# Kernel optimization log

Measured on AMD Instinct MI355X. Metric: run time of the kernel, lower is better.

The kernel has to match this reference:

```python
import jax, jax.numpy as jnp
import numpy as np

N = 120000   # nodes
E = 1200000  # edges
F_IN = 14    # PascalVOC-SP node features
H = 64       # args.hidden
C = 21       # num_classes
EPS = 1e-5


def _glorot(k, shape):
    fan_in = shape[0]
    return jax.random.normal(k, shape, jnp.float32) / np.sqrt(fan_in).astype(np.float32)


def setup_inputs() -> dict:
    key = jax.random.key(0)
    ks = jax.random.split(key, 16)
    inp = {}
    inp['x1'] = jax.random.normal(ks[0], (N, F_IN), jnp.float32)
    inp['edge_index'] = jax.random.randint(ks[1], (2, E), 0, N)
    dims = [(F_IN, H), (H, H), (H, H), (H, H)]
    i = 2
    for l, (din, dout) in enumerate(dims, 1):
        inp[f'Wn{l}'] = _glorot(ks[i], (din, dout)); i += 1
        inp[f'Wr{l}'] = _glorot(ks[i], (din, dout)); i += 1
        inp[f'b{l}'] = jnp.zeros((dout,), jnp.float32)
    for l in (1, 2, 3):
        inp[f'g{l}'] = jnp.ones((H,), jnp.float32)
        inp[f'be{l}'] = jnp.zeros((H,), jnp.float32)
    inp['Wm0'] = _glorot(ks[10], (H, H))
    inp['gm0'] = jnp.ones((H,), jnp.float32)
    inp['bem0'] = jnp.zeros((H,), jnp.float32)
    inp['Wm1'] = _glorot(ks[11], (H, H))
    inp['gm1'] = jnp.ones((H,), jnp.float32)
    inp['bem1'] = jnp.zeros((H,), jnp.float32)
    inp['Wm2'] = _glorot(ks[12], (H, C))
    inp['bm2'] = jnp.zeros((C,), jnp.float32)
    return inp


def _bn(x, g, b):
    # BatchNorm1d forward with batch statistics (train-mode normalization, biased var)
    m = x.mean(axis=0)
    v = x.var(axis=0)
    return (x - m) * jax.lax.rsqrt(v + EPS) * g + b


def _sage(x, src, dst, Wn, Wr, b):
    # PyG SAGEConv (mean aggr): out = mean_neighbors @ Wn + b + x @ Wr
    s = jax.ops.segment_sum(x[src], dst, num_segments=N)        # [N, d]
    cnt = jax.ops.segment_sum(jnp.ones((src.shape[0],), x.dtype), dst, num_segments=N)
    mean = s / jnp.maximum(cnt, 1.0)[:, None]
    return mean @ Wn + b + x @ Wr


def _lrelu(z):
    return jnp.where(z > 0, z, 0.01 * z)


def reference(x1, edge_index, Wn1, Wr1, b1, Wn2, Wr2, b2, Wn3, Wr3, b3, Wn4, Wr4, b4,
              g1, be1, g2, be2, g3, be3, Wm0, gm0, bem0, Wm1, gm1, bem1, Wm2, bm2):
    src, dst = edge_index[0], edge_index[1]
    x = _bn(_lrelu(_sage(x1, src, dst, Wn1, Wr1, b1)), g1, be1)   # conv1 + bano1 (dropout off)
    x = _bn(_lrelu(_sage(x, src, dst, Wn2, Wr2, b2)), g2, be2)    # conv2 + bano2
    x = _bn(jax.nn.relu(_sage(x, src, dst, Wn3, Wr3, b3)), g3, be3)  # conv3 + bano3
    x = _sage(x, src, dst, Wn4, Wr4, b4)                          # conv4
    # mlpRep: Linear(no bias)->BN->ReLU x2, then Linear(bias), no final act
    x = jax.nn.relu(_bn(x @ Wm0, gm0, bem0))
    x = jax.nn.relu(_bn(x @ Wm1, gm1, bem1))
    return x @ Wm2 + bm2
```

## Files before the change

### kernel.cpp

```cpp
#include <hip/hip_runtime.h>

constexpr int NN = 120000;
constexpr int EE = 1200000;
constexpr float EPSV = 1e-5f;
constexpr int NCBLK   = (NN + 127) / 128;
constexpr int NMFMABLK = NN / 64;
constexpr int ASTRIDE = 32;
constexpr int NSLOT = 64;

constexpr int BNODES  = 128;
constexpr int NBUCK   = (NN + BNODES - 1) / BNODES;
constexpr int BSTRIDE = 1536;
constexpr int EPB3    = 4096;
constexpr int NB3     = (EE + EPB3 - 1) / EPB3;
constexpr int NSTATF  = 5*NSLOT*128;

typedef __attribute__((ext_vector_type(8))) short bf8v;
typedef __attribute__((ext_vector_type(4))) float f4v;

__device__ __forceinline__ float bf2f(unsigned short u){
  union { unsigned i; float f; } v; v.i = ((unsigned)u) << 16; return v.f;
}
__device__ __forceinline__ unsigned short f2bf(float f){
  union { float f; unsigned i; } v; v.f = f;
  unsigned u = v.i;
  return (unsigned short)((u + 0x7FFFu + ((u >> 16) & 1u)) >> 16);
}
__device__ __forceinline__ unsigned pack2(float a, float b){
  return (unsigned)f2bf(a) | ((unsigned)f2bf(b) << 16);
}
__device__ __forceinline__ float act_f(float z, int ACT){
  if (ACT == 1) return z > 0.0f ? z : 0.01f*z;
  if (ACT == 2) return fmaxf(z, 0.0f);
  return z;
}
__device__ __forceinline__ void acc8(uint4 u, float& a0, float& a1, float& a2, float& a3,
                                     float& a4, float& a5, float& a6, float& a7){
  a0 += bf2f((unsigned short)(u.x & 0xFFFF)); a1 += bf2f((unsigned short)(u.x >> 16));
  a2 += bf2f((unsigned short)(u.y & 0xFFFF)); a3 += bf2f((unsigned short)(u.y >> 16));
  a4 += bf2f((unsigned short)(u.z & 0xFFFF)); a5 += bf2f((unsigned short)(u.z >> 16));
  a6 += bf2f((unsigned short)(u.w & 0xFFFF)); a7 += bf2f((unsigned short)(u.w >> 16));
}

__global__ __launch_bounds__(512) void k_bucket(const int* __restrict__ src, const int* __restrict__ dst,
                                                int* __restrict__ cursor, unsigned* __restrict__ bucketed,
                                                float* __restrict__ stats){
  __shared__ int hist[NBUCK];
  __shared__ int lstart[NBUCK];
  const int tid = threadIdx.x;
  const int e0  = blockIdx.x * EPB3;
  for (int i = blockIdx.x*512 + tid; i < NSTATF; i += NB3*512) stats[i] = 0.0f;
  for (int i = tid; i < NBUCK; i += 512) hist[i] = 0;
  __syncthreads();

  const bool full = (e0 + EPB3 <= EE);
  if (full){
    #pragma unroll 4
    for (int k = 0; k < EPB3/512; k++){
      int d = dst[e0 + k*512 + tid];
      atomicAdd(&hist[d >> 7], 1);
    }
  } else {
    #pragma unroll 1
    for (int k = 0; k < EPB3/512; k++){
      int e = e0 + k*512 + tid;
      if (e < EE){
        int d = dst[e];
        atomicAdd(&hist[d >> 7], 1);
      }
    }
  }
  __syncthreads();
  for (int i = tid; i < NBUCK; i += 512){
    int h = hist[i];
    lstart[i] = (h > 0) ? atomicAdd(&cursor[i], h) : 0;
  }
  __syncthreads();
  for (int i = tid; i < NBUCK; i += 512) hist[i] = 0;
  __syncthreads();
  #pragma unroll 1
  for (int k = 0; k < EPB3/512; k++){
    int e = e0 + k*512 + tid;
    if (e < EE){
      int d = dst[e];
      int s = src[e];
      int b = d >> 7;
      int r = atomicAdd(&hist[b], 1);
      int idx = lstart[b] + r;
      if (idx < BSTRIDE)
        bucketed[(size_t)b*BSTRIDE + idx] = ((unsigned)s << 7) | (unsigned)(d & 127);
    }
  }
}

__global__ __launch_bounds__(256) void k_buildadj(const unsigned* __restrict__ bucketed,
                                                  const int* __restrict__ cursor,
                                                  int* __restrict__ cnt, int* __restrict__ adj,
                                                  float* __restrict__ invdeg){
  __shared__ alignas(16) int ladj[BNODES*ASTRIDE];
  __shared__ int lcnt[BNODES];
  const int tid = threadIdx.x;
  const int b   = blockIdx.x;
  if (tid < BNODES) lcnt[tid] = 0;
  __syncthreads();
  const int tot = min(cursor[b], BSTRIDE);
  const unsigned* rp = bucketed + (size_t)b*BSTRIDE;
  for (int e = tid; e < tot; e += 256){
    unsigned rec = rp[e];
    int d = (int)(rec & 127u);
    int s = (int)(rec >> 7);
    int p = atomicAdd(&lcnt[d], 1);
    if (p < ASTRIDE) ladj[d*ASTRIDE + p] = s;
  }
  __syncthreads();
  int4* ap = (int4*)(adj + (size_t)b*BNODES*ASTRIDE);
  const int4* lp = (const int4*)ladj;
  #pragma unroll
  for (int i = 0; i < (BNODES*ASTRIDE/4)/256; i++)
    ap[i*256 + tid] = lp[i*256 + tid];
  if (tid < BNODES){
    int c = lcnt[tid];
    int n = b*BNODES + tid;
    cnt[n] = c;
    invdeg[n] = (c > 0) ? (1.0f/(float)c) : -1.0f;
  }
}

__global__ __launch_bounds__(256) void k_gather14(const float* __restrict__ x,
                                                  const int* __restrict__ cnt, const int* __restrict__ adj,
                                                  float* __restrict__ agg){
  const int lane = threadIdx.x & 63;
  const int f = lane & 15, g = lane >> 4;
  const int wave = blockIdx.x*4 + (threadIdx.x >> 6);
  const int nwav = gridDim.x*4;
  for (int n = wave; n < NN; n += nwav){
    int d = min(cnt[n], ASTRIDE);
    const int st = n*ASTRIDE;
    float acc = 0.0f;
    for (int j = g; j < d; j += 4){
      int s = adj[st+j];
      if (f < 14) acc += x[(size_t)s*14 + f];
    }
    acc += __shfl_down(acc, 32);
    acc += __shfl_down(acc, 16);
    if (lane < 14) agg[(size_t)n*14 + lane] = acc;
  }
}

__global__ __launch_bounds__(256) void k_prep_conv_frag(const float* __restrict__ Wn, const float* __restrict__ Wr,
                                                        const float* __restrict__ b, const float* __restrict__ statSlots,
                                                        const float* __restrict__ g, const float* __restrict__ be,
                                                        unsigned short* __restrict__ frag, float* __restrict__ bias2){
  __shared__ float sc[64], sh[64];
  int t = threadIdx.x;
  if (t < 64){
    float sum = 0.0f, sq = 0.0f;
    #pragma unroll 8
    for (int s = 0; s < NSLOT; s++){
      sum += statSlots[s*128 + t];
      sq  += statSlots[s*128 + 64 + t];
    }
    float m = sum * (1.0f/NN);
    float v = sq * (1.0f/NN) - m*m;
    float a = g[t] * rsqrtf(v + EPSV);
    sc[t] = a; sh[t] = be[t] - m*a;
  }
  __syncthreads();
  if (blockIdx.x == 0 && t < 64){
    float accB = b[t], accN = 0.0f;
    for (int k=0;k<64;k++){
      accB += sh[k]*Wr[k*64+t];
      accN += sh[k]*Wn[k*64+t];
    }
    bias2[t]      = accB;
    bias2[64 + t] = accN;
  }
  {
    int idx = blockIdx.x*256 + t;
    int j    = idx & 7;
    int lane = (idx >> 3) & 63;
    int kk   = (idx >> 9) & 1;
    int ct   = (idx >> 10) & 3;
    int mat  = (idx >> 12) & 1;
    int k    = kk*32 + (lane >> 4)*8 + j;
    int col  = ct*16 + (lane & 15);
    const float* W = mat ? Wr : Wn;
    frag[idx] = f2bf(sc[k] * W[k*64 + col]);
  }
}

__global__ __launch_bounds__(256) void k_prep_lin_frag(const float* __restrict__ W,
                                                       unsigned short* __restrict__ frag,
                                                       float* __restrict__ bias2,
                                                       const float* __restrict__ bnSlots,
                                                       float* __restrict__ bnRed){
  int t = threadIdx.x;
  if (blockIdx.x == 0 && t < 128){
    bias2[t] = 0.0f;
    if (bnSlots){
      float s = 0.0f;
      #pragma unroll 8
      for (int sl = 0; sl < NSLOT; sl++) s += bnSlots[sl*128 + t];
      bnRed[t] = s;
    }
  }
  {
    int idx = blockIdx.x*256 + t;
    int j    = idx & 7;
    int lane = (idx >> 3) & 63;
    int kk   = (idx >> 9) & 1;
    int ct   = (idx >> 10) & 3;
    int k    = kk*32 + (lane >> 4)*8 + j;
    int col  = ct*16 + (lane & 15);
    frag[idx] = f2bf(W[k*64 + col]);
  }
}

__global__ __launch_bounds__(64) void k_prep_aff(const float* __restrict__ st,
                                                 const float* __restrict__ g, const float* __restrict__ be,
                                                 float* __restrict__ aff){
  int t = threadIdx.x;
  float s = 0.0f, q = 0.0f;
  #pragma unroll 8
  for (int sl = 0; sl < NSLOT; sl++){
    s += st[sl*128 + t];
    q += st[sl*128 + 64 + t];
  }
  float m = s*(1.0f/NN);
  float v = q*(1.0f/NN) - m*m;
  float a = g[t]*rsqrtf(v+EPSV);
  aff[t]      = a;
  aff[64 + t] = be[t] - m*a;
}

template<int ACT, bool STATS>
__global__ __launch_bounds__(256, 1) void k_gmfma(const unsigned short* __restrict__ X,
                                                  const int* __restrict__ cnt, const int* __restrict__ adj,
                                                  const float* __restrict__ invdeg,
                                                  const unsigned short* __restrict__ frag,
                                                  const float* __restrict__ bias2,
                                                  unsigned short* __restrict__ out,
                                                  float* __restrict__ statsOut){
  __shared__ unsigned short sMean[64*72];
  __shared__ float sst[512];
  const int tid  = threadIdx.x;
  const int lane = tid & 63;
  const int wv   = tid >> 6;
  const int nb0  = blockIdx.x*64;

  {
    const int q8 = lane & 7;
    const int h8 = lane >> 3;
    #pragma unroll
    for (int t8 = 0; t8 < 2; t8++){
      const int row = wv*16 + h8*2 + t8;
      const int n   = nb0 + row;
      const int d   = min(cnt[n], ASTRIDE);
      const int st  = n*ASTRIDE;
      float a0=0,a1=0,a2=0,a3=0,a4=0,a5=0,a6=0,a7=0;
      int j = 0;
      for (; j + 7 < d; j += 8){
        int4 sa = *(const int4*)(adj + st + j);
        int4 sb = *(const int4*)(adj + st + j + 4);
        uint4 u0 = *(const uint4*)(X + (size_t)sa.x*64 + 8*q8);
        uint4 u1 = *(const uint4*)(X + (size_t)sa.y*64 + 8*q8);
        uint4 u2 = *(const uint4*)(X + (size_t)sa.z*64 + 8*q8);
        uint4 u3 = *(const uint4*)(X + (size_t)sa.w*64 + 8*q8);
        uint4 u4 = *(const uint4*)(X + (size_t)sb.x*64 + 8*q8);
        uint4 u5 = *(const uint4*)(X + (size_t)sb.y*64 + 8*q8);
        uint4 u6 = *(const uint4*)(X + (size_t)sb.z*64 + 8*q8);
        uint4 u7 = *(const uint4*)(X + (size_t)sb.w*64 + 8*q8);
        acc8(u0,a0,a1,a2,a3,a4,a5,a6,a7); acc8(u1,a0,a1,a2,a3,a4,a5,a6,a7);
        acc8(u2,a0,a1,a2,a3,a4,a5,a6,a7); acc8(u3,a0,a1,a2,a3,a4,a5,a6,a7);
        acc8(u4,a0,a1,a2,a3,a4,a5,a6,a7); acc8(u5,a0,a1,a2,a3,a4,a5,a6,a7);
        acc8(u6,a0,a1,a2,a3,a4,a5,a6,a7); acc8(u7,a0,a1,a2,a3,a4,a5,a6,a7);
      }
      for (; j + 3 < d; j += 4){
        int4 sa = *(const int4*)(adj + st + j);
        uint4 u0 = *(const uint4*)(X + (size_t)sa.x*64 + 8*q8);
        uint4 u1 = *(const uint4*)(X + (size_t)sa.y*64 + 8*q8);
        uint4 u2 = *(const uint4*)(X + (size_t)sa.z*64 + 8*q8);
        uint4 u3 = *(const uint4*)(X + (size_t)sa.w*64 + 8*q8);
        acc8(u0,a0,a1,a2,a3,a4,a5,a6,a7); acc8(u1,a0,a1,a2,a3,a4,a5,a6,a7);
        acc8(u2,a0,a1,a2,a3,a4,a5,a6,a7); acc8(u3,a0,a1,a2,a3,a4,a5,a6,a7);
      }
      for (; j < d; j++){
        int s = adj[st + j];
        uint4 u = *(const uint4*)(X + (size_t)s*64 + 8*q8);
        acc8(u,a0,a1,a2,a3,a4,a5,a6,a7);
      }
      float iv = fmaxf(invdeg[n], 0.0f);
      uint4 o;
      o.x = pack2(a0*iv, a1*iv);
      o.y = pack2(a2*iv, a3*iv);
      o.z = pack2(a4*iv, a5*iv);
      o.w = pack2(a6*iv, a7*iv);
      *(uint4*)(sMean + row*72 + 8*q8) = o;
    }
  }

  const bf8v* fp = (const bf8v*)frag;
  bf8v wn[4][2], wr[4][2];
  #pragma unroll
  for (int ct=0;ct<4;ct++){
    #pragma unroll
    for (int kk=0;kk<2;kk++){
      wn[ct][kk] = fp[((0*4+ct)*2+kk)*64 + lane];
      wr[ct][kk] = fp[((1*4+ct)*2+kk)*64 + lane];
    }
  }
  const int m  = lane & 15;
  const int kq = lane >> 4;
  const size_t arow = (size_t)(nb0 + wv*16 + m)*64;
  bf8v ax0 = *(const bf8v*)(X + arow + kq*8);
  bf8v ax1 = *(const bf8v*)(X + arow + 32 + kq*8);
  __syncthreads();
  bf8v am0 = *(const bf8v*)(sMean + (wv*16 + m)*72 + kq*8);
  bf8v am1 = *(const bf8v*)(sMean + (wv*16 + m)*72 + 32 + kq*8);

  f4v acc[4];
  #pragma unroll
  for (int ct=0;ct<4;ct++){
    f4v c = {0.0f,0.0f,0.0f,0.0f};
    c = __builtin_amdgcn_mfma_f32_16x16x32_bf16(am0, wn[ct][0], c, 0,0,0);
    c = __builtin_amdgcn_mfma_f32_16x16x32_bf16(am1, wn[ct][1], c, 0,0,0);
    c = __builtin_amdgcn_mfma_f32_16x16x32_bf16(ax0, wr[ct][0], c, 0,0,0);
    c = __builtin_amdgcn_mfma_f32_16x16x32_bf16(ax1, wr[ct][1], c, 0,0,0);
    acc[ct] = c;
  }

  const int col = lane & 15;
  float bb[4], bg[4];
  #pragma unroll
  for (int ct=0;ct<4;ct++){
    bb[ct] = bias2[ct*16 + col];
    bg[ct] = bias2[64 + ct*16 + col];
  }
  float ls[4] = {0,0,0,0}, lq[4] = {0,0,0,0};
  #pragma unroll
  for (int r=0;r<4;r++){
    const int node = nb0 + wv*16 + (lane>>4)*4 + r;
    float gadd = (invdeg[node] > 0.0f) ? 1.0f : 0.0f;
    #pragma unroll
    for (int ct=0;ct<4;ct++){
      float z = acc[ct][r] + bb[ct] + gadd * bg[ct];
      z = act_f(z, ACT);
      out[(size_t)node*64 + ct*16 + col] = f2bf(z);
      if (STATS){ ls[ct] += z; lq[ct] = fmaf(z, z, lq[ct]); }
    }
  }
  if constexpr (STATS){
    #pragma unroll
    for (int ct=0;ct<4;ct++){
      float s = ls[ct]; s += __shfl_down(s, 32); s += __shfl_down(s, 16);
      float q = lq[ct]; q += __shfl_down(q, 32); q += __shfl_down(q, 16);
      if (kq == 0){
        sst[wv*128 + ct*16 + col]      = s;
        sst[wv*128 + 64 + ct*16 + col] = q;
      }
    }
    __syncthreads();
    if (tid < 128){
      float v = sst[tid] + sst[128+tid] + sst[256+tid] + sst[384+tid];
      atomicAdd(&statsOut[(blockIdx.x & (NSLOT-1))*128 + tid], v);
    }
  }
}

template<int ACT, bool STATS, bool BNA>
__global__ __launch_bounds__(256, 1) void k_mfma_lin(const unsigned short* __restrict__ Ax,
                                                     const unsigned short* __restrict__ frag,
                                                     const float* __restrict__ bias2,
                                                     unsigned short* __restrict__ out,
                                                     float* __restrict__ statsOut,
                                                     const float* __restrict__ bnRed,
                                                     const float* __restrict__ bnG,
                                                     const float* __restrict__ bnB){
  __shared__ float sst[512];
  const int lane = threadIdx.x & 63;
  const int wv   = threadIdx.x >> 6;
  const int n0   = (blockIdx.x*4 + wv)*16;
  const int m    = lane & 15;
  const int kq   = lane >> 4;

  const bf8v* fp = (const bf8v*)frag;
  bf8v wr[4][2];
  #pragma unroll
  for (int ct=0;ct<4;ct++){
    #pragma unroll
    for (int kk=0;kk<2;kk++) wr[ct][kk] = fp[(ct*2+kk)*64 + lane];
  }

  const size_t arow = (size_t)(n0 + m)*64;
  bf8v ax0 = *(const bf8v*)(Ax + arow + kq*8);
  bf8v ax1 = *(const bf8v*)(Ax + arow + 32 + kq*8);
  if constexpr (BNA){
    #pragma unroll
    for (int j=0;j<8;j++){
      int k0 = kq*8 + j, k1 = 32 + kq*8 + j;
      float m0 = bnRed[k0]*(1.0f/NN);
      float v0 = bnRed[64+k0]*(1.0f/NN) - m0*m0;
      float a0 = bnG[k0]*rsqrtf(v0+EPSV);
      float b0 = bnB[k0] - m0*a0;
      ax0[j] = (short)f2bf(fmaxf(fmaf(a0, bf2f((unsigned short)ax0[j]), b0), 0.0f));
      float m1 = bnRed[k1]*(1.0f/NN);
      float v1 = bnRed[64+k1]*(1.0f/NN) - m1*m1;
      float a1 = bnG[k1]*rsqrtf(v1+EPSV);
      float b1 = bnB[k1] - m1*a1;
      ax1[j] = (short)f2bf(fmaxf(fmaf(a1, bf2f((unsigned short)ax1[j]), b1), 0.0f));
    }
  }

  f4v acc[4];
  #pragma unroll
  for (int ct=0;ct<4;ct++){
    f4v c = {0.0f,0.0f,0.0f,0.0f};
    c = __builtin_amdgcn_mfma_f32_16x16x32_bf16(ax0, wr[ct][0], c, 0,0,0);
    c = __builtin_amdgcn_mfma_f32_16x16x32_bf16(ax1, wr[ct][1], c, 0,0,0);
    acc[ct] = c;
  }

  const int col = lane & 15;
  float bb[4];
  #pragma unroll
  for (int ct=0;ct<4;ct++) bb[ct] = bias2[ct*16 + col];
  float ls[4] = {0,0,0,0}, lq[4] = {0,0,0,0};
  #pragma unroll
  for (int r=0;r<4;r++){
    const int node = n0 + (lane>>4)*4 + r;
    #pragma unroll
    for (int ct=0;ct<4;ct++){
      float z = act_f(acc[ct][r] + bb[ct], ACT);
      out[(size_t)node*64 + ct*16 + col] = f2bf(z);
      if (STATS){ ls[ct] += z; lq[ct] = fmaf(z, z, lq[ct]); }
    }
  }
  if constexpr (STATS){
    #pragma unroll
    for (int ct=0;ct<4;ct++){
      float s = ls[ct]; s += __shfl_down(s, 32); s += __shfl_down(s, 16);
      float q = lq[ct]; q += __shfl_down(q, 32); q += __shfl_down(q, 16);
      if (kq == 0){
        sst[wv*128 + ct*16 + col]      = s;
        sst[wv*128 + 64 + ct*16 + col] = q;
      }
    }
    __syncthreads();
    if (threadIdx.x < 128){
      float v = sst[threadIdx.x] + sst[128+threadIdx.x] + sst[256+threadIdx.x] + sst[384+threadIdx.x];
      atomicAdd(&statsOut[(blockIdx.x & (NSLOT-1))*128 + threadIdx.x], v);
    }
  }
}

__global__ __launch_bounds__(128, 1) void k_gemm_conv14(const float* __restrict__ agg, const float* __restrict__ x,
                                                        const float* __restrict__ invdeg,
                                                        const float* __restrict__ Wn, const float* __restrict__ Wr,
                                                        const float* __restrict__ b,
                                                        unsigned short* __restrict__ out, float* __restrict__ statsOut){
  constexpr int DIN = 14, RS = 15;
  __shared__ float sRow[128*RS];
  const int tid = threadIdx.x;
  const int lane = tid & 63;
  const int n0  = blockIdx.x*128;
  const int n   = n0 + tid;

  {
    const float* gp = agg + (size_t)n0*DIN;
    for (int i = tid; i < 128*DIN; i += 128){
      int r = i / DIN, c = i - r*DIN;
      sRow[r*RS + c] = (n0 + r < NN) ? gp[i] : 0.0f;
    }
  }
  __syncthreads();

  float accA0[32], accA1[32];
  #pragma unroll
  for (int jj=0;jj<32;jj++){ accA0[jj]=0.0f; accA1[jj]=0.0f; }

  #pragma unroll 1
  for (int k=0;k<DIN;k++){
    float rv = sRow[tid*RS + k];
    const float* wr = Wn + k*64;
    #pragma unroll
    for (int jj=0;jj<32;jj++) accA0[jj] = fmaf(wr[jj],    rv, accA0[jj]);
    #pragma unroll
    for (int jj=0;jj<32;jj++) accA1[jj] = fmaf(wr[32+jj], rv, accA1[jj]);
  }
  __syncthreads();
  {
    const float* gp = x + (size_t)n0*DIN;
    for (int i = tid; i < 128*DIN; i += 128){
      int r = i / DIN, c = i - r*DIN;
      sRow[r*RS + c] = (n0 + r < NN) ? gp[i] : 0.0f;
    }
  }
  __syncthreads();

  const bool valid = (n < NN);
  float iv = valid ? invdeg[n] : -1.0f;
  const bool gate = iv > 0.0f;
  #pragma unroll
  for (int jj=0;jj<32;jj++){
    accA0[jj] = gate ? accA0[jj]*iv : 0.0f;
    accA1[jj] = gate ? accA1[jj]*iv : 0.0f;
  }

  #pragma unroll 1
  for (int k=0;k<DIN;k++){
    float rv = sRow[tid*RS + k];
    const float* wr = Wr + k*64;
    #pragma unroll
    for (int jj=0;jj<32;jj++) accA0[jj] = fmaf(wr[jj],    rv, accA0[jj]);
    #pragma unroll
    for (int jj=0;jj<32;jj++) accA1[jj] = fmaf(wr[32+jj], rv, accA1[jj]);
  }

  uint2* o2 = (uint2*)(out + (size_t)n*64);
  float vs[64], vq[64];
  #pragma unroll
  for (int q=0;q<8;q++){
    float z0 = valid ? act_f(accA0[4*q+0]+b[4*q+0],1) : 0.0f;
    float z1 = valid ? act_f(accA0[4*q+1]+b[4*q+1],1) : 0.0f;
    float z2 = valid ? act_f(accA0[4*q+2]+b[4*q+2],1) : 0.0f;
    float z3 = valid ? act_f(accA0[4*q+3]+b[4*q+3],1) : 0.0f;
    vs[4*q+0] = z0; vs[4*q+1] = z1; vs[4*q+2] = z2; vs[4*q+3] = z3;
    if (valid){ uint2 t; t.x = pack2(z0,z1); t.y = pack2(z2,z3); o2[q] = t; }
  }
  #pragma unroll
  for (int q=0;q<8;q++){
    float z0 = valid ? act_f(accA1[4*q+0]+b[32+4*q+0],1) : 0.0f;
    float z1 = valid ? act_f(accA1[4*q+1]+b[32+4*q+1],1) : 0.0f;
    float z2 = valid ? act_f(accA1[4*q+2]+b[32+4*q+2],1) : 0.0f;
    float z3 = valid ? act_f(accA1[4*q+3]+b[32+4*q+3],1) : 0.0f;
    vs[32+4*q+0] = z0; vs[32+4*q+1] = z1; vs[32+4*q+2] = z2; vs[32+4*q+3] = z3;
    if (valid){ uint2 t; t.x = pack2(z0,z1); t.y = pack2(z2,z3); o2[8+q] = t; }
  }
  #pragma unroll
  for (int j=0;j<64;j++) vq[j] = vs[j]*vs[j];

  #pragma unroll
  for (int k=0;k<6;k++){
    const bool keep1 = ((lane >> k) & 1) != 0;
    const int half = 64 >> (k+1);
    #pragma unroll
    for (int i=0;i<half;i++){
      float sa = vs[2*i], sb = vs[2*i+1];
      float qa = vq[2*i], qb = vq[2*i+1];
      float skeep = keep1 ? sb : sa;
      float ssend = keep1 ? sa : sb;
      float qkeep = keep1 ? qb : qa;
      float qsend = keep1 ? qa : qb;
      vs[i] = skeep + __shfl_xor(ssend, 1<<k);
      vq[i] = qkeep + __shfl_xor(qsend, 1<<k);
    }
  }
  const int slot = (blockIdx.x & (NSLOT-1))*128;
  atomicAdd(&statsOut[slot + lane],      vs[0]);
  atomicAdd(&statsOut[slot + 64 + lane], vq[0]);
}

__global__ __launch_bounds__(256, 1) void k_lin21(const unsigned short* __restrict__ x,
                                                  const float* __restrict__ W, const float* __restrict__ bias,
                                                  const float* __restrict__ aff,
                                                  float* __restrict__ out){
  __shared__ float sW[64*21];
  __shared__ float sAff[128];
  const int tid = threadIdx.x;
  if (tid < 128) sAff[tid] = aff[tid];
  for (int i = tid; i < 64*21; i += 256) sW[i] = W[i];
  __syncthreads();

  const int p  = tid & 3;
  const int nl = tid >> 2;
  const int n  = blockIdx.x*64 + nl;
  const bool valid = (n < NN);
  const int k0 = p*16;

  uint4 u0 = {0,0,0,0}, u1 = {0,0,0,0};
  if (valid){
    const unsigned short* rp = x + (size_t)n*64 + k0;
    u0 = *(const uint4*)(rp);
    u1 = *(const uint4*)(rp + 8);
  }
  float f[16];
  f[0]=bf2f((unsigned short)(u0.x&0xFFFF)); f[1]=bf2f((unsigned short)(u0.x>>16));
  f[2]=bf2f((unsigned short)(u0.y&0xFFFF)); f[3]=bf2f((unsigned short)(u0.y>>16));
  f[4]=bf2f((unsigned short)(u0.z&0xFFFF)); f[5]=bf2f((unsigned short)(u0.z>>16));
  f[6]=bf2f((unsigned short)(u0.w&0xFFFF)); f[7]=bf2f((unsigned short)(u0.w>>16));
  f[8]=bf2f((unsigned short)(u1.x&0xFFFF)); f[9]=bf2f((unsigned short)(u1.x>>16));
  f[10]=bf2f((unsigned short)(u1.y&0xFFFF)); f[11]=bf2f((unsigned short)(u1.y>>16));
  f[12]=bf2f((unsigned short)(u1.z&0xFFFF)); f[13]=bf2f((unsigned short)(u1.z>>16));
  f[14]=bf2f((unsigned short)(u1.w&0xFFFF)); f[15]=bf2f((unsigned short)(u1.w>>16));
  #pragma unroll
  for (int j=0;j<16;j++)
    f[j] = fmaxf(fmaf(sAff[k0+j], f[j], sAff[64+k0+j]), 0.0f);

  float a[21];
  #pragma unroll
  for (int jj=0;jj<21;jj++) a[jj] = 0.0f;
  #pragma unroll
  for (int k=0;k<16;k++){
    const float* wr = sW + (k0+k)*21;
    float rv = f[k];
    #pragma unroll
    for (int jj=0;jj<21;jj++) a[jj] = fmaf(wr[jj], rv, a[jj]);
  }
  #pragma unroll
  for (int jj=0;jj<21;jj++){
    a[jj] += __shfl_xor(a[jj], 1);
    a[jj] += __shfl_xor(a[jj], 2);
  }
  if (valid){
    const int c0 = p*6;
    const int ce = (p == 3) ? 21 : c0 + 6;
    float* op = out + (size_t)n*21;
    #pragma unroll 6
    for (int jj=c0; jj<ce; jj++) op[jj] = a[jj] + bias[jj];
  }
}

extern "C" void kernel_launch(void* const* d_in, const int* in_sizes, int n_in,
                              void* d_out, int out_size, void* d_ws, size_t ws_size,
                              hipStream_t stream){
  const float* x1  = (const float*)d_in[0];
  const int*   ei  = (const int*)d_in[1];
  const int* srcp = ei;
  const int* dstp = ei + EE;
  const float *Wn1=(const float*)d_in[2],  *Wr1=(const float*)d_in[3],  *b1=(const float*)d_in[4];
  const float *Wn2=(const float*)d_in[5],  *Wr2=(const float*)d_in[6],  *b2=(const float*)d_in[7];
  const float *Wn3=(const float*)d_in[8],  *Wr3=(const float*)d_in[9],  *b3=(const float*)d_in[10];
  const float *Wn4=(const float*)d_in[11], *Wr4=(const float*)d_in[12], *b4=(const float*)d_in[13];
  const float *g1=(const float*)d_in[14], *be1=(const float*)d_in[15];
  const float *g2=(const float*)d_in[16], *be2=(const float*)d_in[17];
  const float *g3=(const float*)d_in[18], *be3=(const float*)d_in[19];
  const float *Wm0=(const float*)d_in[20], *gm0=(const float*)d_in[21], *bem0=(const float*)d_in[22];
  const float *Wm1=(const float*)d_in[23], *gm1=(const float*)d_in[24], *bem1=(const float*)d_in[25];
  const float *Wm2=(const float*)d_in[26], *bm2=(const float*)d_in[27];
  float* out = (float*)d_out;

  char* ws = (char*)d_ws;
  int*   cnt     = (int*)(ws);
  float* invdeg  = (float*)(ws + (1ull<<20));
  int*   adj     = (int*)(ws + (2ull<<20));
  float* agg14   = (float*)(ws + (18ull<<20));
  unsigned short* hA   = (unsigned short*)(ws + (25ull<<20));
  unsigned short* hB   = (unsigned short*)(ws + (41ull<<20));
  float* stats   = (float*)(ws + (57ull<<20));
  float* bnRed   = (float*)(ws + (57ull<<20) + 192*1024);
  float* aff5    = (float*)(ws + (57ull<<20) + 224*1024);
  unsigned short* fragC = (unsigned short*)(ws + (58ull<<20));
  float* bias2C  = (float*)(ws + (58ull<<20) + 65536);
  unsigned short* fragL = (unsigned short*)(ws + (59ull<<20));
  float* bias2L  = (float*)(ws + (59ull<<20) + 65536);
  unsigned* bucketed = (unsigned*)(ws + (25ull<<20));
  int* cursor        = (int*)(ws + (25ull<<20) + (6ull<<20));

  float* S1 = stats;
  float* S2 = stats + NSLOT*128;
  float* S3 = stats + 2*NSLOT*128;
  float* S4 = stats + 3*NSLOT*128;
  float* S5 = stats + 4*NSLOT*128;

  hipMemsetAsync(cursor, 0, NBUCK*sizeof(int), stream);
  k_bucket  <<<NB3,  512,0,stream>>>(srcp, dstp, cursor, bucketed, stats);
  k_buildadj<<<NBUCK,256,0,stream>>>(bucketed, cursor, cnt, adj, invdeg);

  k_gather14<<<2048,256,0,stream>>>(x1, cnt, adj, agg14);
  k_gemm_conv14<<<NCBLK,128,0,stream>>>(agg14,x1,invdeg,Wn1,Wr1,b1,hA,S1);

  k_prep_conv_frag<<<32,256,0,stream>>>(Wn2,Wr2,b2,S1,g1,be1,fragC,bias2C);
  k_gmfma<1,true><<<NMFMABLK,256,0,stream>>>(hA,cnt,adj,invdeg,fragC,bias2C,hB,S2);

  k_prep_conv_frag<<<32,256,0,stream>>>(Wn3,Wr3,b3,S2,g2,be2,fragC,bias2C);
  k_gmfma<2,true><<<NMFMABLK,256,0,stream>>>(hB,cnt,adj,invdeg,fragC,bias2C,hA,S3);

  k_prep_conv_frag<<<32,256,0,stream>>>(Wn4,Wr4,b4,S3,g3,be3,fragC,bias2C);
  k_gmfma<0,false><<<NMFMABLK,256,0,stream>>>(hA,cnt,adj,invdeg,fragC,bias2C,hB,nullptr);

  k_prep_lin_frag<<<16,256,0,stream>>>(Wm0, fragL, bias2L, nullptr, nullptr);
  k_mfma_lin<0,true,false><<<NMFMABLK,256,0,stream>>>(hB,fragL,bias2L,hA,S4,nullptr,nullptr,nullptr);

  k_prep_lin_frag<<<16,256,0,stream>>>(Wm1, fragL, bias2L, S4, bnRed);
  k_mfma_lin<0,true,true><<<NMFMABLK,256,0,stream>>>(hA,fragL,bias2L,hB,S5,bnRed,gm0,bem0);

  k_prep_aff<<<1,64,0,stream>>>(S5, gm1, bem1, aff5);
  k_lin21<<<NMFMABLK,256,0,stream>>>(hB,Wm2,bm2,aff5,out);
}
```

Before: 398.3 us.

## Fuse layer-1 neighbor gather into conv1 kernel using bf16-packed padded features

Converts the 14-wide fp32 input features to a padded bf16 layout of 32 bytes per row inside the bucketing kernel. The separate gather kernel is removed, and conv1 now does its own per-thread neighbor mean aggregation before the dense transform. This drops one launch and the agg14 intermediate round trip, and halves gather bytes. In exchange, each thread walks its node's adjacency serially, which may hurt latency hiding in a kernel limited to 128 threads with one block, and bf16 rounding of the input features lowers precision.

```diff
diff --git a/kernel.cpp b/kernel.cpp
--- a/kernel.cpp
+++ b/kernel.cpp
@@ -44,12 +44,20 @@
 
 __global__ __launch_bounds__(512) void k_bucket(const int* __restrict__ src, const int* __restrict__ dst,
                                                 int* __restrict__ cursor, unsigned* __restrict__ bucketed,
-                                                float* __restrict__ stats){
+                                                float* __restrict__ stats,
+                                                const float* __restrict__ x, unsigned* __restrict__ xb){
   __shared__ int hist[NBUCK];
   __shared__ int lstart[NBUCK];
   const int tid = threadIdx.x;
   const int e0  = blockIdx.x * EPB3;
   for (int i = blockIdx.x*512 + tid; i < NSTATF; i += NB3*512) stats[i] = 0.0f;
+  for (int i = blockIdx.x*512 + tid; i < NN*8; i += NB3*512){
+    int n = i >> 3, j = i & 7;
+    int c0 = 2*j, c1 = 2*j + 1;
+    float f0 = (c0 < 14) ? x[(size_t)n*14 + c0] : 0.0f;
+    float f1 = (c1 < 14) ? x[(size_t)n*14 + c1] : 0.0f;
+    xb[i] = pack2(f0, f1);
+  }
   for (int i = tid; i < NBUCK; i += 512) hist[i] = 0;
   __syncthreads();
 
@@ -123,27 +131,6 @@
     int n = b*BNODES + tid;
     cnt[n] = c;
     invdeg[n] = (c > 0) ? (1.0f/(float)c) : -1.0f;
-  }
-}
-
-__global__ __launch_bounds__(256) void k_gather14(const float* __restrict__ x,
-                                                  const int* __restrict__ cnt, const int* __restrict__ adj,
-                                                  float* __restrict__ agg){
-  const int lane = threadIdx.x & 63;
-  const int f = lane & 15, g = lane >> 4;
-  const int wave = blockIdx.x*4 + (threadIdx.x >> 6);
-  const int nwav = gridDim.x*4;
-  for (int n = wave; n < NN; n += nwav){
-    int d = min(cnt[n], ASTRIDE);
-    const int st = n*ASTRIDE;
-    float acc = 0.0f;
-    for (int j = g; j < d; j += 4){
-      int s = adj[st+j];
-      if (f < 14) acc += x[(size_t)s*14 + f];
-    }
-    acc += __shfl_down(acc, 32);
-    acc += __shfl_down(acc, 16);
-    if (lane < 14) agg[(size_t)n*14 + lane] = acc;
   }
 }
 
@@ -453,62 +440,71 @@
   }
 }
 
-__global__ __launch_bounds__(128, 1) void k_gemm_conv14(const float* __restrict__ agg, const float* __restrict__ x,
-                                                        const float* __restrict__ invdeg,
-                                                        const float* __restrict__ Wn, const float* __restrict__ Wr,
-                                                        const float* __restrict__ b,
-                                                        unsigned short* __restrict__ out, float* __restrict__ statsOut){
+__global__ __launch_bounds__(128, 1) void k_conv1(const unsigned* __restrict__ xb, const float* __restrict__ x,
+                                                  const int* __restrict__ cnt, const int* __restrict__ adj,
+                                                  const float* __restrict__ invdeg,
+                                                  const float* __restrict__ Wn, const float* __restrict__ Wr,
+                                                  const float* __restrict__ b,
+                                                  unsigned short* __restrict__ out, float* __restrict__ statsOut){
   constexpr int DIN = 14, RS = 15;
-  __shared__ float sRow[128*RS];
+  __shared__ float sMean[128*RS];
+  __shared__ float sX[128*RS];
   const int tid = threadIdx.x;
   const int lane = tid & 63;
   const int n0  = blockIdx.x*128;
   const int n   = n0 + tid;
-
-  {
-    const float* gp = agg + (size_t)n0*DIN;
-    for (int i = tid; i < 128*DIN; i += 128){
-      int r = i / DIN, c = i - r*DIN;
-      sRow[r*RS + c] = (n0 + r < NN) ? gp[i] : 0.0f;
-    }
-  }
-  __syncthreads();
-
-  float accA0[32], accA1[32];
-  #pragma unroll
-  for (int jj=0;jj<32;jj++){ accA0[jj]=0.0f; accA1[jj]=0.0f; }
-
-  #pragma unroll 1
-  for (int k=0;k<DIN;k++){
-    float rv = sRow[tid*RS + k];
-    const float* wr = Wn + k*64;
-    #pragma unroll
-    for (int jj=0;jj<32;jj++) accA0[jj] = fmaf(wr[jj],    rv, accA0[jj]);
-    #pragma unroll
-    for (int jj=0;jj<32;jj++) accA1[jj] = fmaf(wr[32+jj], rv, accA1[jj]);
-  }
-  __syncthreads();
+  const bool valid = (n < NN);
+
   {
     const float* gp = x + (size_t)n0*DIN;
     for (int i = tid; i < 128*DIN; i += 128){
       int r = i / DIN, c = i - r*DIN;
-      sRow[r*RS + c] = (n0 + r < NN) ? gp[i] : 0.0f;
-    }
-  }
-  __syncthreads();
-
-  const bool valid = (n < NN);
-  float iv = valid ? invdeg[n] : -1.0f;
-  const bool gate = iv > 0.0f;
-  #pragma unroll
-  for (int jj=0;jj<32;jj++){
-    accA0[jj] = gate ? accA0[jj]*iv : 0.0f;
-    accA1[jj] = gate ? accA1[jj]*iv : 0.0f;
-  }
+      sX[r*RS + c] = (n0 + r < NN) ? gp[i] : 0.0f;
+    }
+  }
+
+  {
+    float mm[14];
+    #pragma unroll
+    for (int j=0;j<14;j++) mm[j] = 0.0f;
+    const int d  = valid ? min(cnt[n], ASTRIDE) : 0;
+    const int st = n*ASTRIDE;
+    #pragma unroll 2
+    for (int j=0;j<d;j++){
+      int s = adj[st+j];
+      const uint4* rp = (const uint4*)(xb + s*8);
+      uint4 u0 = rp[0], u1 = rp[1];
+      mm[0]+=bf2f((unsigned short)(u0.x&0xFFFF)); mm[1]+=bf2f((unsigned short)(u0.x>>16));
+      mm[2]+=bf2f((unsigned short)(u0.y&0xFFFF)); mm[3]+=bf2f((unsigned short)(u0.y>>16));
+      mm[4]+=bf2f((unsigned short)(u0.z&0xFFFF)); mm[5]+=bf2f((unsigned short)(u0.z>>16));
+      mm[6]+=bf2f((unsigned short)(u0.w&0xFFFF)); mm[7]+=bf2f((unsigned short)(u0.w>>16));
+      mm[8]+=bf2f((unsigned short)(u1.x&0xFFFF)); mm[9]+=bf2f((unsigned short)(u1.x>>16));
+      mm[10]+=bf2f((unsigned short)(u1.y&0xFFFF)); mm[11]+=bf2f((unsigned short)(u1.y>>16));
+      mm[12]+=bf2f((unsigned short)(u1.z&0xFFFF)); mm[13]+=bf2f((unsigned short)(u1.z>>16));
+    }
+    float iv = valid ? invdeg[n] : -1.0f;
+    float gate = (iv > 0.0f) ? iv : 0.0f;
+    #pragma unroll
+    for (int j=0;j<14;j++) sMean[tid*RS + j] = mm[j]*gate;
+  }
+  __syncthreads();
+
+  float accA0[32], accA1[32];
+  #pragma unroll
+  for (int jj=0;jj<32;jj++){ accA0[jj]=0.0f; accA1[jj]=0.0f; }
 
   #pragma unroll 1
   for (int k=0;k<DIN;k++){
-    float rv = sRow[tid*RS + k];
+    float rv = sMean[tid*RS + k];
+    const float* wr = Wn + k*64;
+    #pragma unroll
+    for (int jj=0;jj<32;jj++) accA0[jj] = fmaf(wr[jj],    rv, accA0[jj]);
+    #pragma unroll
+    for (int jj=0;jj<32;jj++) accA1[jj] = fmaf(wr[32+jj], rv, accA1[jj]);
+  }
+  #pragma unroll 1
+  for (int k=0;k<DIN;k++){
+    float rv = sX[tid*RS + k];
     const float* wr = Wr + k*64;
     #pragma unroll
     for (int jj=0;jj<32;jj++) accA0[jj] = fmaf(wr[jj],    rv, accA0[jj]);
@@ -643,7 +639,6 @@
   int*   cnt     = (int*)(ws);
   float* invdeg  = (float*)(ws + (1ull<<20));
   int*   adj     = (int*)(ws + (2ull<<20));
-  float* agg14   = (float*)(ws + (18ull<<20));
   unsigned short* hA   = (unsigned short*)(ws + (25ull<<20));
   unsigned short* hB   = (unsigned short*)(ws + (41ull<<20));
   float* stats   = (float*)(ws + (57ull<<20));
@@ -653,6 +648,7 @@
   float* bias2C  = (float*)(ws + (58ull<<20) + 65536);
   unsigned short* fragL = (unsigned short*)(ws + (59ull<<20));
   float* bias2L  = (float*)(ws + (59ull<<20) + 65536);
+  unsigned* xb   = (unsigned*)(ws + (60ull<<20));
   unsigned* bucketed = (unsigned*)(ws + (25ull<<20));
   int* cursor        = (int*)(ws + (25ull<<20) + (6ull<<20));
 
@@ -663,11 +659,10 @@
   float* S5 = stats + 4*NSLOT*128;
 
   hipMemsetAsync(cursor, 0, NBUCK*sizeof(int), stream);
-  k_bucket  <<<NB3,  512,0,stream>>>(srcp, dstp, cursor, bucketed, stats);
+  k_bucket  <<<NB3,  512,0,stream>>>(srcp, dstp, cursor, bucketed, stats, x1, xb);
   k_buildadj<<<NBUCK,256,0,stream>>>(bucketed, cursor, cnt, adj, invdeg);
 
-  k_gather14<<<2048,256,0,stream>>>(x1, cnt, adj, agg14);
-  k_gemm_conv14<<<NCBLK,128,0,stream>>>(agg14,x1,invdeg,Wn1,Wr1,b1,hA,S1);
+  k_conv1<<<NCBLK,128,0,stream>>>(xb,x1,cnt,adj,invdeg,Wn1,Wr1,b1,hA,S1);
 
   k_prep_conv_frag<<<32,256,0,stream>>>(Wn2,Wr2,b2,S1,g1,be1,fragC,bias2C);
   k_gmfma<1,true><<<NMFMABLK,256,0,stream>>>(hA,cnt,adj,invdeg,fragC,bias2C,hB,S2);
```

After: 362.4 us. -9.0%, faster.
